# Performance work log

Hardware: AMD Instinct MI355X
Metric: run time of the kernel (lower is better)

The kernel has to match this reference:

```python
import jax, jax.numpy as jnp
import numpy as np

# Dims: C = 8*8*4 = 256 input channels, O = 8*8*8 = 512 output channels,
# space_rank = 4, TT ranks = (4, 16, 16).

def setup_inputs() -> dict:
    key = jax.random.key(0)
    ks = jax.random.split(key, 6)
    inp = jax.random.normal(ks[0], (32, 256, 32, 32), dtype=jnp.float32)
    # space_factor: (space_rank, 1, kH, kW)
    space_factor = jax.random.normal(ks[1], (4, 1, 3, 3), dtype=jnp.float32) * 0.3
    # factors[i]: (in_i, rank_i, rank_{i+1}, out_i)
    factor0 = jax.random.normal(ks[2], (8, 4, 16, 8), dtype=jnp.float32) * 0.1
    factor1 = jax.random.normal(ks[3], (8, 16, 16, 8), dtype=jnp.float32) * 0.08
    # last_factor: (in_last, rank_last, out_last)
    last_factor = jax.random.normal(ks[4], (4, 16, 8), dtype=jnp.float32) * 0.1
    bias = jax.random.uniform(ks[5], (512,), dtype=jnp.float32, minval=-0.02, maxval=0.02)
    return {"input": inp, "space_factor": space_factor, "factor0": factor0,
            "factor1": factor1, "last_factor": last_factor, "bias": bias}


def reference(input, space_factor, factor0, factor1, last_factor, bias):
    B, C, H, W = input.shape
    sr = space_factor.shape[0]
    # Depthwise conv: each of the C channels convolved with the same
    # `space_rank` filters (torch repeat along out-channel dim + groups=C).
    w = jnp.tile(space_factor, (C, 1, 1, 1))  # (C*sr, 1, kH, kW)
    y = jax.lax.conv_general_dilated(
        input, w, window_strides=(1, 1), padding=[(1, 1), (1, 1)],
        feature_group_count=C,
        dimension_numbers=("NCHW", "OIHW", "NCHW"))  # (B, C*sr, H', W')
    Hp, Wp = y.shape[2], y.shape[3]
    # (B, n0, n1, n2, sr, H', W') with (n0,n1,n2) = input_chanel_shape
    t = y.reshape(B, 8, 8, 4, sr, Hp, Wp)
    # Contract the tiny TT cores first (optimal order found by tn.contractors.optimal):
    # chain: (n0, n1, n2, r0, o0, o1, o2) -- only ~0.5M elements.
    chain = jnp.einsum("apqx,bqry,crz->abcpxyz", factor0, factor1, last_factor)
    # One big contraction over (n0, n1, n2, r0): effectively a GEMM
    # (B*H'*W', C*sr) x (C*sr, O).
    out = jnp.einsum("nabcphw,abcpxyz->nxyzhw", t, chain)
    out = out.reshape(B, 512, Hp, Wp)
    return out + bias[None, :, None, None]
```

## Files before the change

### kernel.cpp

```cpp
#include <hip/hip_runtime.h>

typedef unsigned short ushort_t;
typedef __attribute__((ext_vector_type(8))) short bf16x8;
typedef __attribute__((ext_vector_type(8))) unsigned short ushort8;
typedef __attribute__((ext_vector_type(4))) float f32x4;

__device__ __forceinline__ unsigned short f2bf(float f) {
  union { float f; unsigned u; } x; x.f = f;
  unsigned r = x.u + 0x7FFFu + ((x.u >> 16) & 1u);
  return (unsigned short)(r >> 16);
}

__global__ void chain_g_kernel(const float* __restrict__ f1,
                               const float* __restrict__ lf,
                               float* __restrict__ g) {
  int idx = blockIdx.x * 256 + threadIdx.x;
  int z = idx & 7, c = (idx >> 3) & 3, y = (idx >> 5) & 7,
      q = (idx >> 8) & 15, b = idx >> 12;
  float s = 0.f;
  #pragma unroll
  for (int r = 0; r < 16; ++r)
    s += f1[((b * 16 + q) * 16 + r) * 8 + y] * lf[(c * 16 + r) * 8 + z];
  g[idx] = s;
}

__global__ void chain_kernel(const float* __restrict__ f0,
                             const float* __restrict__ g,
                             ushort_t* __restrict__ chainT) {
  int idx = blockIdx.x * 256 + threadIdx.x;
  int k = idx & 1023, o = idx >> 10;
  int p = k & 3, c = (k >> 2) & 3, b = (k >> 4) & 7, a = k >> 7;
  int z = o & 7, y = (o >> 3) & 7, x = o >> 6;
  float s = 0.f;
  #pragma unroll
  for (int q = 0; q < 16; ++q)
    s += f0[((a * 4 + p) * 16 + q) * 8 + x] *
         g[(((b * 16 + q) * 8 + y) * 4 + c) * 8 + z];
  chainT[idx] = f2bf(s);
}

__global__ __launch_bounds__(256) void conv_kernel(const float* __restrict__ in,
                                                   const float* __restrict__ sf,
                                                   ushort_t* __restrict__ t) {
  __shared__ float in_lds[64][244];
  __shared__ float sf_l[36];
  int bid = blockIdx.x;
  int cq = bid & 3, h4 = (bid >> 2) & 7, n = bid >> 5;
  int h0 = h4 * 4;
  int tid = threadIdx.x;
  if (tid < 36) sf_l[tid] = sf[tid];
  for (int e = tid; e < 384; e += 256) {
    int ch = e / 6, r = e % 6;
    in_lds[ch][r * 40 + 3] = 0.f;
    in_lds[ch][r * 40 + 36] = 0.f;
  }
  const float* inb = in + ((size_t)n * 256 + cq * 64) * 1024;
  #pragma unroll
  for (int i = 0; i < 12; ++i) {
    int e = tid + i * 256;
    int ch = e / 48, rem = e % 48;
    int r = rem >> 3, w4 = rem & 7;
    int hh = h0 - 1 + r;
    float4 v = make_float4(0.f, 0.f, 0.f, 0.f);
    if (hh >= 0 && hh < 32)
      v = *(const float4*)&inb[(size_t)ch * 1024 + hh * 32 + w4 * 4];
    *(float4*)&in_lds[ch][r * 40 + 4 + w4 * 4] = v;
  }
  __syncthreads();
  float sfr[36];
  #pragma unroll
  for (int i = 0; i < 36; ++i) sfr[i] = sf_l[i];
  int w = tid >> 3, gg = tid & 7;
  size_t m0 = (size_t)n * 1024 + (size_t)h0 * 32 + w;
  #pragma unroll
  for (int j = 0; j < 4; ++j) {
    float acc[4][2][4];
    #pragma unroll
    for (int b = 0; b < 2; ++b) {
      int ch = j * 16 + gg * 2 + b;
      float vals[6][3];
      #pragma unroll
      for (int r = 0; r < 6; ++r)
        #pragma unroll
        for (int dw = 0; dw < 3; ++dw)
          vals[r][dw] = in_lds[ch][r * 40 + 3 + w + dw];
      #pragma unroll
      for (int hh = 0; hh < 4; ++hh)
        #pragma unroll
        for (int p = 0; p < 4; ++p) {
          float s = 0.f;
          #pragma unroll
          for (int dr = 0; dr < 3; ++dr)
            #pragma unroll
            for (int dw = 0; dw < 3; ++dw)
              s += vals[hh + dr][dw] * sfr[p * 9 + dr * 3 + dw];
          acc[hh][b][p] = s;
        }
    }
    #pragma unroll
    for (int hh = 0; hh < 4; ++hh) {
      ushort8 outv;
      #pragma unroll
      for (int b = 0; b < 2; ++b)
        #pragma unroll
        for (int p = 0; p < 4; ++p) outv[b * 4 + p] = f2bf(acc[hh][b][p]);
      *(ushort8*)&t[(m0 + hh * 32) * 1024 + (size_t)(cq * 256 + j * 64 + gg * 8)] = outv;
    }
  }
}

#define AS1 __attribute__((address_space(1)))
#define AS3 __attribute__((address_space(3)))
#define BARRIER __builtin_amdgcn_s_barrier()
#define VMCNT4  asm volatile("s_waitcnt vmcnt(4)" ::: "memory")
#define VMCNT0  asm volatile("s_waitcnt vmcnt(0)" ::: "memory")

__global__ __launch_bounds__(512, 2) void gemm_kernel(const ushort_t* __restrict__ tA,
                                                      const ushort_t* __restrict__ tB,
                                                      const float* __restrict__ bias,
                                                      float* __restrict__ out) {
  __shared__ __align__(16) ushort_t smem[65536];
  int tid = threadIdx.x;
  int bid = blockIdx.x;
  int wg = (bid & 7) * 32 + (bid >> 3);
  int tile_m = (wg >> 1) * 256;
  int tile_n = (wg & 1) * 256;

  int lane = tid & 63, wv = tid >> 6;
  int wm2 = wv >> 2, wn4 = wv & 3;
  int lr = lane & 15, kg = lane >> 4;
  int kph0 = ((kg * 8) ^ ((lane & 7) * 8));
  int kph1 = ((32 + kg * 8) ^ ((lane & 7) * 8));
  int arow = wm2 * 128 + lr;
  int brow = wn4 * 64 + lr;

  int srow = tid >> 3;
  int scol = ((tid & 7) ^ (srow & 7)) * 8;
  const ushort_t* sA = tA + (size_t)(tile_m + srow) * 1024 + scol;
  const ushort_t* sB = tB + (size_t)(tile_n + srow) * 1024 + scol;

#define STAGE_A(buf, koff, h)                                                                  \
  __builtin_amdgcn_global_load_lds((const AS1 void*)(sA + (size_t)((h)*128) * 1024 + (koff)),  \
      (AS3 void*)&smem[(buf)*16384 + (h)*8192 + tid*8], 16, 0, 0);                             \
  __builtin_amdgcn_global_load_lds((const AS1 void*)(sA + (size_t)((h)*128+64) * 1024 + (koff)),\
      (AS3 void*)&smem[(buf)*16384 + (h)*8192 + 4096 + tid*8], 16, 0, 0);
#define STAGE_B(buf, koff, h)                                                                  \
  __builtin_amdgcn_global_load_lds((const AS1 void*)(sB + (size_t)((h)*128) * 1024 + (koff)),  \
      (AS3 void*)&smem[32768 + (buf)*16384 + (h)*8192 + tid*8], 16, 0, 0);                     \
  __builtin_amdgcn_global_load_lds((const AS1 void*)(sB + (size_t)((h)*128+64) * 1024 + (koff)),\
      (AS3 void*)&smem[32768 + (buf)*16384 + (h)*8192 + 4096 + tid*8], 16, 0, 0);

#define READ_A(dst, mbase, buf)                                                                \
  _Pragma("unroll")                                                                            \
  for (int mf = 0; mf < 4; ++mf) {                                                             \
    dst[mf][0] = *(const bf16x8*)&smem[(buf)*16384 + (arow + (mbase) + mf*16)*64 + kph0];      \
    dst[mf][1] = *(const bf16x8*)&smem[(buf)*16384 + (arow + (mbase) + mf*16)*64 + kph1];      \
  }
#define READ_B(dst, nbase, buf)                                                                \
  _Pragma("unroll")                                                                            \
  for (int nf = 0; nf < 2; ++nf) {                                                             \
    dst[nf][0] = *(const bf16x8*)&smem[32768 + (buf)*16384 + (brow + (nbase) + nf*16)*64 + kph0];\
    dst[nf][1] = *(const bf16x8*)&smem[32768 + (buf)*16384 + (brow + (nbase) + nf*16)*64 + kph1];\
  }
#define Q_MFMA(AF, BF, MB, NB)                                                                 \
  __builtin_amdgcn_s_setprio(1);                                                              \
  _Pragma("unroll")                                                                            \
  for (int mf = 0; mf < 4; ++mf)                                                               \
    _Pragma("unroll")                                                                          \
    for (int nf = 0; nf < 2; ++nf)                                                             \
      _Pragma("unroll")                                                                        \
      for (int ks = 0; ks < 2; ++ks)                                                           \
        acc[(MB) + mf][(NB) + nf] = __builtin_amdgcn_mfma_f32_16x16x32_bf16(                   \
            AF[mf][ks], BF[nf][ks], acc[(MB) + mf][(NB) + nf], 0, 0, 0);                       \
  __builtin_amdgcn_s_setprio(0);

  f32x4 acc[8][4];
  #pragma unroll
  for (int i = 0; i < 8; ++i)
    #pragma unroll
    for (int j = 0; j < 4; ++j) acc[i][j] = (f32x4){0.f, 0.f, 0.f, 0.f};

  bf16x8 a1[4][2], a2[4][2], b1[2][2], b2[2][2];

  STAGE_A(0, 0, 0) STAGE_A(0, 0, 1) STAGE_B(0, 0, 0) STAGE_B(0, 0, 1)
  STAGE_A(1, 64, 0) STAGE_A(1, 64, 1)
  VMCNT4; BARRIER;

#define ITER(I_, FULL)                                                                         \
  {                                                                                            \
    int k1 = (2*(I_)+1)*64, k2 = (2*(I_)+2)*64, k3 = (2*(I_)+3)*64;                            \
                                                                 \
    VMCNT4;                                                                                    \
    READ_A(a1, 0, 0) READ_B(b1, 0, 0)                                                          \
    STAGE_B(1, k1, 0) BARRIER;                                                                 \
    Q_MFMA(a1, b1, 0, 0) BARRIER;                                                              \
                                                                                       \
    READ_B(b2, 32, 0) STAGE_B(1, k1, 1) BARRIER;                                               \
    Q_MFMA(a1, b2, 0, 2) BARRIER;                                                              \
                                                                                       \
    READ_A(a2, 64, 0) if (FULL) { STAGE_A(0, k2, 0) } BARRIER;                                 \
    Q_MFMA(a2, b2, 4, 2) BARRIER;                                                              \
                                                                                       \
    if (FULL) { STAGE_A(0, k2, 1) } BARRIER;                                                   \
    Q_MFMA(a2, b1, 4, 0) BARRIER;                                                              \
                                                                  \
    if (FULL) { VMCNT4; } else { VMCNT0; }                                                     \
    READ_A(a1, 0, 1) READ_B(b1, 0, 1)                                                          \
    if (FULL) { STAGE_B(0, k2, 0) } BARRIER;                                                   \
    Q_MFMA(a1, b1, 0, 0) BARRIER;                                                              \
                                                                                       \
    READ_B(b2, 32, 1) if (FULL) { STAGE_B(0, k2, 1) } BARRIER;                                 \
    Q_MFMA(a1, b2, 0, 2) BARRIER;                                                              \
                                                                                       \
    READ_A(a2, 64, 1) if (FULL) { STAGE_A(1, k3, 0) } BARRIER;                                 \
    Q_MFMA(a2, b2, 4, 2) BARRIER;                                                              \
                                                                                       \
    if (FULL) { STAGE_A(1, k3, 1) } BARRIER;                                                   \
    Q_MFMA(a2, b1, 4, 0) BARRIER;                                                              \
  }

  for (int I = 0; I < 7; ++I) ITER(I, 1)
  ITER(7, 0)
#undef ITER

  #pragma unroll
  for (int mf = 0; mf < 8; ++mf)
    #pragma unroll
    for (int nf = 0; nf < 4; ++nf) {
      int m = tile_m + wm2 * 128 + mf * 16 + kg * 4;
      int o = tile_n + wn4 * 64 + nf * 16 + lr;
      float bv = bias[o];
      f32x4 v = acc[mf][nf];
      v[0] += bv; v[1] += bv; v[2] += bv; v[3] += bv;
      *(f32x4*)&out[(size_t)(m >> 10) * 524288 + (size_t)o * 1024 + (size_t)(m & 1023)] = v;
    }
}

extern "C" void kernel_launch(void* const* d_in, const int* in_sizes, int n_in,
                              void* d_out, int out_size, void* d_ws, size_t ws_size,
                              hipStream_t stream) {
  (void)in_sizes; (void)n_in; (void)out_size; (void)ws_size;
  const float* in   = (const float*)d_in[0];
  const float* sf   = (const float*)d_in[1];
  const float* f0   = (const float*)d_in[2];
  const float* f1   = (const float*)d_in[3];
  const float* lf   = (const float*)d_in[4];
  const float* bias = (const float*)d_in[5];
  float* out = (float*)d_out;

  char* ws = (char*)d_ws;
  ushort_t* t      = (ushort_t*)ws;
  ushort_t* chainT = (ushort_t*)(ws + 67108864);
  float*    g      = (float*)(ws + 67108864 + 1048576);

  hipLaunchKernelGGL(chain_g_kernel, dim3(128),  dim3(256), 0, stream, f1, lf, g);
  hipLaunchKernelGGL(chain_kernel,   dim3(2048), dim3(256), 0, stream, f0, g, chainT);
  hipLaunchKernelGGL(conv_kernel,    dim3(1024), dim3(256), 0, stream, in, sf, t);
  hipLaunchKernelGGL(gemm_kernel,    dim3(256),  dim3(512), 0, stream, t, chainT, bias, out);
}
```

Before: 75.39 us.

## Shrink GEMM tiles to 128x128 with more blocks and a lighter pipeline

The GEMM tile drops from 256x256 to 128x128, giving 1024 workgroups instead of 256 and halving LDS use so more blocks can be resident per CU. Each wave now holds a 32x64 accumulator instead of 128x64, and the wait counts and barriers are rearranged to match (explicit lgkmcnt waits, vmcnt(2)). The bias is loaded before the main loop. The aim is better CU occupancy and load balance across the MI355X (256 tiles on 256 CUs left little latency hiding), at the cost of less operand reuse and more global/L2 traffic.

```diff
diff --git a/kernel.cpp b/kernel.cpp
--- a/kernel.cpp
+++ b/kernel.cpp
@@ -111,28 +111,29 @@
 
 #define AS1 __attribute__((address_space(1)))
 #define AS3 __attribute__((address_space(3)))
-#define BARRIER __builtin_amdgcn_s_barrier()
-#define VMCNT4  asm volatile("s_waitcnt vmcnt(4)" ::: "memory")
-#define VMCNT0  asm volatile("s_waitcnt vmcnt(0)" ::: "memory")
-
-__global__ __launch_bounds__(512, 2) void gemm_kernel(const ushort_t* __restrict__ tA,
+#define BARRIER  __builtin_amdgcn_s_barrier()
+#define LGKMCNT0 asm volatile("s_waitcnt lgkmcnt(0)" ::: "memory")
+#define VMCNT2   asm volatile("s_waitcnt vmcnt(2)" ::: "memory")
+#define VMCNT0   asm volatile("s_waitcnt vmcnt(0)" ::: "memory")
+
+__global__ __launch_bounds__(512, 4) void gemm_kernel(const ushort_t* __restrict__ tA,
                                                       const ushort_t* __restrict__ tB,
                                                       const float* __restrict__ bias,
                                                       float* __restrict__ out) {
-  __shared__ __align__(16) ushort_t smem[65536];
+  __shared__ __align__(16) ushort_t smem[32768];
   int tid = threadIdx.x;
   int bid = blockIdx.x;
-  int wg = (bid & 7) * 32 + (bid >> 3);
-  int tile_m = (wg >> 1) * 256;
-  int tile_n = (wg & 1) * 256;
+  int wg = (bid & 7) * 128 + (bid >> 3);
+  int tile_m = (wg >> 2) * 128;
+  int tile_n = (wg & 3) * 128;
 
   int lane = tid & 63, wv = tid >> 6;
-  int wm2 = wv >> 2, wn4 = wv & 3;
+  int wm = (wv >> 1) * 32, wn = (wv & 1) * 64;
   int lr = lane & 15, kg = lane >> 4;
   int kph0 = ((kg * 8) ^ ((lane & 7) * 8));
   int kph1 = ((32 + kg * 8) ^ ((lane & 7) * 8));
-  int arow = wm2 * 128 + lr;
-  int brow = wn4 * 64 + lr;
+  int arow = wm + lr;
+  int brow = wn + lr;
 
   int srow = tid >> 3;
   int scol = ((tid & 7) ^ (srow & 7)) * 8;
@@ -140,83 +141,83 @@
   const ushort_t* sB = tB + (size_t)(tile_n + srow) * 1024 + scol;
 
 #define STAGE_A(buf, koff, h)                                                                  \
-  __builtin_amdgcn_global_load_lds((const AS1 void*)(sA + (size_t)((h)*128) * 1024 + (koff)),  \
-      (AS3 void*)&smem[(buf)*16384 + (h)*8192 + tid*8], 16, 0, 0);                             \
-  __builtin_amdgcn_global_load_lds((const AS1 void*)(sA + (size_t)((h)*128+64) * 1024 + (koff)),\
-      (AS3 void*)&smem[(buf)*16384 + (h)*8192 + 4096 + tid*8], 16, 0, 0);
+  __builtin_amdgcn_global_load_lds((const AS1 void*)(sA + (size_t)((h)*64) * 1024 + (koff)),   \
+      (AS3 void*)&smem[(buf)*8192 + (h)*4096 + tid*8], 16, 0, 0);
 #define STAGE_B(buf, koff, h)                                                                  \
-  __builtin_amdgcn_global_load_lds((const AS1 void*)(sB + (size_t)((h)*128) * 1024 + (koff)),  \
-      (AS3 void*)&smem[32768 + (buf)*16384 + (h)*8192 + tid*8], 16, 0, 0);                     \
-  __builtin_amdgcn_global_load_lds((const AS1 void*)(sB + (size_t)((h)*128+64) * 1024 + (koff)),\
-      (AS3 void*)&smem[32768 + (buf)*16384 + (h)*8192 + 4096 + tid*8], 16, 0, 0);
-
-#define READ_A(dst, mbase, buf)                                                                \
-  _Pragma("unroll")                                                                            \
-  for (int mf = 0; mf < 4; ++mf) {                                                             \
-    dst[mf][0] = *(const bf16x8*)&smem[(buf)*16384 + (arow + (mbase) + mf*16)*64 + kph0];      \
-    dst[mf][1] = *(const bf16x8*)&smem[(buf)*16384 + (arow + (mbase) + mf*16)*64 + kph1];      \
-  }
+  __builtin_amdgcn_global_load_lds((const AS1 void*)(sB + (size_t)((h)*64) * 1024 + (koff)),   \
+      (AS3 void*)&smem[16384 + (buf)*8192 + (h)*4096 + tid*8], 16, 0, 0);
+
+#define READ_A1(dst, buf)                                                                      \
+  dst[0] = *(const bf16x8*)&smem[(buf)*8192 + (arow)*64 + kph0];                               \
+  dst[1] = *(const bf16x8*)&smem[(buf)*8192 + (arow)*64 + kph1];
+#define READ_A2(dst, buf)                                                                      \
+  dst[0] = *(const bf16x8*)&smem[(buf)*8192 + (arow + 16)*64 + kph0];                          \
+  dst[1] = *(const bf16x8*)&smem[(buf)*8192 + (arow + 16)*64 + kph1];
 #define READ_B(dst, nbase, buf)                                                                \
   _Pragma("unroll")                                                                            \
   for (int nf = 0; nf < 2; ++nf) {                                                             \
-    dst[nf][0] = *(const bf16x8*)&smem[32768 + (buf)*16384 + (brow + (nbase) + nf*16)*64 + kph0];\
-    dst[nf][1] = *(const bf16x8*)&smem[32768 + (buf)*16384 + (brow + (nbase) + nf*16)*64 + kph1];\
+    dst[nf][0] = *(const bf16x8*)&smem[16384 + (buf)*8192 + (brow + (nbase) + nf*16)*64 + kph0];\
+    dst[nf][1] = *(const bf16x8*)&smem[16384 + (buf)*8192 + (brow + (nbase) + nf*16)*64 + kph1];\
   }
 #define Q_MFMA(AF, BF, MB, NB)                                                                 \
   __builtin_amdgcn_s_setprio(1);                                                              \
   _Pragma("unroll")                                                                            \
-  for (int mf = 0; mf < 4; ++mf)                                                               \
+  for (int nf = 0; nf < 2; ++nf)                                                               \
     _Pragma("unroll")                                                                          \
-    for (int nf = 0; nf < 2; ++nf)                                                             \
-      _Pragma("unroll")                                                                        \
-      for (int ks = 0; ks < 2; ++ks)                                                           \
-        acc[(MB) + mf][(NB) + nf] = __builtin_amdgcn_mfma_f32_16x16x32_bf16(                   \
-            AF[mf][ks], BF[nf][ks], acc[(MB) + mf][(NB) + nf], 0, 0, 0);                       \
+    for (int ks = 0; ks < 2; ++ks)                                                             \
+      acc[MB][(NB) + nf] = __builtin_amdgcn_mfma_f32_16x16x32_bf16(                            \
+          AF[ks], BF[nf][ks], acc[MB][(NB) + nf], 0, 0, 0);                                    \
   __builtin_amdgcn_s_setprio(0);
 
-  f32x4 acc[8][4];
-  #pragma unroll
-  for (int i = 0; i < 8; ++i)
+  f32x4 acc[2][4];
+  #pragma unroll
+  for (int i = 0; i < 2; ++i)
     #pragma unroll
     for (int j = 0; j < 4; ++j) acc[i][j] = (f32x4){0.f, 0.f, 0.f, 0.f};
 
-  bf16x8 a1[4][2], a2[4][2], b1[2][2], b2[2][2];
+  float bv[4];
+  #pragma unroll
+  for (int nf = 0; nf < 4; ++nf) bv[nf] = bias[tile_n + wn + nf * 16 + lr];
+
+  bf16x8 a1[2], a2[2], b1[2][2], b2[2][2];
 
   STAGE_A(0, 0, 0) STAGE_A(0, 0, 1) STAGE_B(0, 0, 0) STAGE_B(0, 0, 1)
   STAGE_A(1, 64, 0) STAGE_A(1, 64, 1)
-  VMCNT4; BARRIER;
+  VMCNT2; BARRIER;
 
 #define ITER(I_, FULL)                                                                         \
   {                                                                                            \
     int k1 = (2*(I_)+1)*64, k2 = (2*(I_)+2)*64, k3 = (2*(I_)+3)*64;                            \
-                                                                 \
-    VMCNT4;                                                                                    \
-    READ_A(a1, 0, 0) READ_B(b1, 0, 0)                                                          \
-    STAGE_B(1, k1, 0) BARRIER;                                                                 \
+                \
+    READ_A1(a1, 0) READ_A2(a2, 0) READ_B(b1, 0, 0)                                             \
+    STAGE_B(1, k1, 0) BARRIER; LGKMCNT0;                                                       \
     Q_MFMA(a1, b1, 0, 0) BARRIER;                                                              \
                                                                                        \
-    READ_B(b2, 32, 0) STAGE_B(1, k1, 1) BARRIER;                                               \
+    READ_B(b2, 32, 0) STAGE_B(1, k1, 1) BARRIER; LGKMCNT0;                                     \
     Q_MFMA(a1, b2, 0, 2) BARRIER;                                                              \
                                                                                        \
-    READ_A(a2, 64, 0) if (FULL) { STAGE_A(0, k2, 0) } BARRIER;                                 \
-    Q_MFMA(a2, b2, 4, 2) BARRIER;                                                              \
-                                                                                       \
+    if (FULL) { STAGE_A(0, k2, 0) } BARRIER;                                                   \
+    Q_MFMA(a2, b2, 1, 2) BARRIER;                                                              \
+                                    \
     if (FULL) { STAGE_A(0, k2, 1) } BARRIER;                                                   \
-    Q_MFMA(a2, b1, 4, 0) BARRIER;                                                              \
-                                                                  \
-    if (FULL) { VMCNT4; } else { VMCNT0; }                                                     \
-    READ_A(a1, 0, 1) READ_B(b1, 0, 1)                                                          \
-    if (FULL) { STAGE_B(0, k2, 0) } BARRIER;                                                   \
+    Q_MFMA(a2, b1, 1, 0)                                                                       \
+    if (FULL) { VMCNT2; } else { VMCNT0; }                                                     \
+    BARRIER;                                                                                   \
+                                                                           \
+    READ_A1(a1, 1) READ_A2(a2, 1) READ_B(b1, 0, 1)                                             \
+    if (FULL) { STAGE_B(0, k2, 0) } BARRIER; LGKMCNT0;                                         \
     Q_MFMA(a1, b1, 0, 0) BARRIER;                                                              \
                                                                                        \
-    READ_B(b2, 32, 1) if (FULL) { STAGE_B(0, k2, 1) } BARRIER;                                 \
+    READ_B(b2, 32, 1) if (FULL) { STAGE_B(0, k2, 1) } BARRIER; LGKMCNT0;                       \
     Q_MFMA(a1, b2, 0, 2) BARRIER;                                                              \
                                                                                        \
-    READ_A(a2, 64, 1) if (FULL) { STAGE_A(1, k3, 0) } BARRIER;                                 \
-    Q_MFMA(a2, b2, 4, 2) BARRIER;                                                              \
-                                                                                       \
+    if (FULL) { STAGE_A(1, k3, 0) } BARRIER;                                                   \
+    Q_MFMA(a2, b2, 1, 2) BARRIER;                                                              \
+                                    \
     if (FULL) { STAGE_A(1, k3, 1) } BARRIER;                                                   \
-    Q_MFMA(a2, b1, 4, 0) BARRIER;                                                              \
+    Q_MFMA(a2, b1, 1, 0)                                                                       \
+    if (FULL) { VMCNT2; }                                                                      \
+    BARRIER;                                                                                   \
   }
 
   for (int I = 0; I < 7; ++I) ITER(I, 1)
@@ -224,14 +225,13 @@
 #undef ITER
 
   #pragma unroll
-  for (int mf = 0; mf < 8; ++mf)
+  for (int mf = 0; mf < 2; ++mf)
     #pragma unroll
     for (int nf = 0; nf < 4; ++nf) {
-      int m = tile_m + wm2 * 128 + mf * 16 + kg * 4;
-      int o = tile_n + wn4 * 64 + nf * 16 + lr;
-      float bv = bias[o];
+      int m = tile_m + wm + mf * 16 + kg * 4;
+      int o = tile_n + wn + nf * 16 + lr;
       f32x4 v = acc[mf][nf];
-      v[0] += bv; v[1] += bv; v[2] += bv; v[3] += bv;
+      v[0] += bv[nf]; v[1] += bv[nf]; v[2] += bv[nf]; v[3] += bv[nf];
       *(f32x4*)&out[(size_t)(m >> 10) * 524288 + (size_t)o * 1024 + (size_t)(m & 1023)] = v;
     }
 }
@@ -256,5 +256,5 @@
   hipLaunchKernelGGL(chain_g_kernel, dim3(128),  dim3(256), 0, stream, f1, lf, g);
   hipLaunchKernelGGL(chain_kernel,   dim3(2048), dim3(256), 0, stream, f0, g, chainT);
   hipLaunchKernelGGL(conv_kernel,    dim3(1024), dim3(256), 0, stream, in, sf, t);
-  hipLaunchKernelGGL(gemm_kernel,    dim3(256),  dim3(512), 0, stream, t, chainT, bias, out);
-}
+  hipLaunchKernelGGL(gemm_kernel,    dim3(1024), dim3(512), 0, stream, t, chainT, bias, out);
+}
```

Result: slower. 78.51 us (+4.1%).
